# Optimization experiments

Hardware: AMD Instinct MI355X
Metric: run time of the kernel (lower is better)

## Reference

```python
import jax, jax.numpy as jnp
import numpy as np

B, S, H, L = 64, 512, 768, 9


def setup_inputs() -> dict:
    key = jax.random.key(0)
    ks = jax.random.split(key, 8)
    hidden = jax.random.normal(ks[0], (B, S, H), jnp.float32)
    lengths = jax.random.randint(ks[1], (B,), S // 2, S + 1)
    attention_mask = (jnp.arange(S)[None, :] < lengths[:, None]).astype(jnp.int32)
    labels = jax.random.randint(ks[2], (B, S), 0, L)
    # sprinkle some -100 ignore labels like HF datasets do
    ignore = jax.random.uniform(ks[3], (B, S)) < 0.05
    labels = jnp.where(ignore, -100, labels)
    W = jax.random.normal(ks[4], (H, L), jnp.float32) * 0.02
    b = jnp.zeros((L,), jnp.float32)
    start_transitions = jax.random.uniform(ks[5], (L,), jnp.float32, -0.1, 0.1)
    end_transitions = jax.random.uniform(ks[6], (L,), jnp.float32, -0.1, 0.1)
    transitions = jax.random.uniform(ks[7], (L, L), jnp.float32, -0.1, 0.1)
    return dict(hidden=hidden, attention_mask=attention_mask, labels=labels, W=W, b=b,
                start_transitions=start_transitions, end_transitions=end_transitions,
                transitions=transitions)


def _crf_numerator(emissions, tags, maskf, start_t, end_t, trans):
    # score of the gold tag sequence (torchcrf _compute_score)
    first = start_t[tags[:, 0]] + jnp.take_along_axis(emissions[:, 0], tags[:, 0:1], axis=1)[:, 0]
    em = jnp.take_along_axis(emissions, tags[..., None], axis=2)[..., 0]      # [B,S]
    tr = trans[tags[:, :-1], tags[:, 1:]]                                     # [B,S-1]
    score = first + jnp.sum((em[:, 1:] + tr) * maskf[:, 1:], axis=1)
    last_idx = (jnp.sum(maskf, axis=1).astype(jnp.int32) - 1)
    last_tags = jnp.take_along_axis(tags, last_idx[:, None], axis=1)[:, 0]
    return score + end_t[last_tags]


def _crf_lognorm(emissions, maskf, start_t, end_t, trans):
    # forward algorithm (torchcrf _compute_normalizer) as a lax.scan
    score0 = start_t[None, :] + emissions[:, 0]                               # [B,L]
    em_seq = jnp.transpose(emissions[:, 1:], (1, 0, 2))                       # [S-1,B,L]
    m_seq = maskf[:, 1:].T                                                    # [S-1,B]

    def step(score, xs):
        em_t, m_t = xs
        nxt = jax.nn.logsumexp(score[:, :, None] + trans[None] + em_t[:, None, :], axis=1)
        return jnp.where(m_t[:, None] > 0, nxt, score), None

    score, _ = jax.lax.scan(step, score0, (em_seq, m_seq))
    return jax.nn.logsumexp(score + end_t[None, :], axis=1)


def _viterbi(emissions, maskf, start_t, end_t, trans):
    score0 = start_t[None, :] + emissions[:, 0]                               # [B,L]
    em_seq = jnp.transpose(emissions[:, 1:], (1, 0, 2))
    m_seq = maskf[:, 1:].T

    def step(score, xs):
        em_t, m_t = xs
        cand = score[:, :, None] + trans[None]                                # [B,L,L]
        bp = jnp.argmax(cand, axis=1)                                         # [B,L]
        nxt = jnp.max(cand, axis=1) + em_t
        return jnp.where(m_t[:, None] > 0, nxt, score), bp

    score, history = jax.lax.scan(step, score0, (em_seq, m_seq))              # history [S-1,B,L]
    best_last = jnp.argmax(score + end_t[None, :], axis=1)                    # [B]

    def back(cur, xs):
        bp_t, m_t = xs
        prev = jnp.where(m_t > 0, jnp.take_along_axis(bp_t, cur[:, None], axis=1)[:, 0], cur)
        return prev, prev

    _, tags_rev = jax.lax.scan(back, best_last, (history[::-1], m_seq[::-1]))
    tags = jnp.concatenate([tags_rev[::-1].T, best_last[:, None]], axis=1)    # [B,S]
    return tags


def reference(hidden, attention_mask, labels, W, b, start_transitions, end_transitions, transitions):
    maskf = attention_mask.astype(hidden.dtype)                               # [B,S]
    logits = jnp.einsum('bsh,hl->bsl', hidden, W) + b                         # [B,S,L]
    safe_labels = jnp.where(labels == -100, 0, labels)
    num = _crf_numerator(logits, safe_labels, maskf, start_transitions, end_transitions, transitions)
    den = _crf_lognorm(logits, maskf, start_transitions, end_transitions, transitions)
    loss = -jnp.mean(num - den)                                               # -crf(..., reduction='mean')
    tags = _viterbi(logits, maskf, start_transitions, end_transitions, transitions)
    fake_logits = jax.nn.one_hot(tags, L, dtype=logits.dtype) * maskf[..., None]
    return loss, fake_logits
```

## Files before the change

kernel.cpp:

```cpp
#include <hip/hip_runtime.h>
#include <hip/hip_bf16.h>
#include <stdint.h>

constexpr int BB  = 64;
constexpr int SS  = 512;
constexpr int HH  = 768;
constexpr int NL  = 9;
constexpr int NROWS = BB * SS;
constexpr int EMN   = SS * NL;
constexpr int NSEG  = 8;
constexpr float NEG  = -1e30f;

__device__ __forceinline__ float readlane_f(float v, int lane) {
  union { float f; int i; } u;
  u.f = v;
  u.i = __builtin_amdgcn_readlane(u.i, lane);
  return u.f;
}

__device__ __forceinline__ float max3f(float a, float b, float c) {
  float d;
  asm("v_max3_f32 %0, %1, %2, %3" : "=v"(d) : "v"(a), "v"(b), "v"(c));
  return d;
}

__device__ __forceinline__ float max9f(const float* c) {
  return max3f(max3f(c[0], c[1], c[2]),
               max3f(c[3], c[4], c[5]),
               max3f(c[6], c[7], c[8]));
}

__global__ __launch_bounds__(256, 2) void logits_kernel(
    const float* __restrict__ hidden, const float* __restrict__ W,
    const float* __restrict__ bias, const int* __restrict__ mask,
    float* __restrict__ logits, int* __restrict__ lens,
    float* __restrict__ out) {
  const int lane = threadIdx.x & 63;
  const int wid  = blockIdx.x * 4 + (threadIdx.x >> 6);

  if (blockIdx.x == 0 && threadIdx.x == 0) out[0] = 0.0f;

  if (blockIdx.x < 64 && threadIdx.x < 64) {
    const int4* mp = (const int4*)(mask + blockIdx.x * SS);
    const int4 a = mp[threadIdx.x];
    const int4 c = mp[threadIdx.x + 64];
    int lsum = a.x + a.y + a.z + a.w + c.x + c.y + c.z + c.w;
#pragma unroll
    for (int off = 32; off >= 1; off >>= 1) lsum += __shfl_xor(lsum, off, 64);
    if (threadIdx.x == 0) lens[blockIdx.x] = lsum;
  }

  float w[3][4][NL];
#pragma unroll
  for (int j = 0; j < 3; ++j)
#pragma unroll
    for (int k = 0; k < 4; ++k) {
      const int r = lane * 4 + j * 256 + k;
#pragma unroll
      for (int l = 0; l < NL; ++l) w[j][k][l] = W[r * NL + l];
    }
  const float my_bias = (lane < NL) ? bias[lane] : 0.0f;

  float4 h[4][3];
#pragma unroll
  for (int r = 0; r < 4; ++r) {
    const float4* hp = (const float4*)(hidden + (size_t)(wid + r * 8192) * HH);
#pragma unroll
    for (int j = 0; j < 3; ++j) h[r][j] = hp[lane + j * 64];
  }
  float acc[4][NL];
#pragma unroll
  for (int r = 0; r < 4; ++r)
#pragma unroll
    for (int l = 0; l < NL; ++l) acc[r][l] = 0.0f;
#pragma unroll
  for (int r = 0; r < 4; ++r)
#pragma unroll
    for (int j = 0; j < 3; ++j)
#pragma unroll
      for (int l = 0; l < NL; ++l)
        acc[r][l] += h[r][j].x * w[j][0][l] + h[r][j].y * w[j][1][l] +
                     h[r][j].z * w[j][2][l] + h[r][j].w * w[j][3][l];
#pragma unroll
  for (int off = 32; off >= 1; off >>= 1)
#pragma unroll
    for (int r = 0; r < 4; ++r)
#pragma unroll
      for (int l = 0; l < NL; ++l)
        acc[r][l] += __shfl_xor(acc[r][l], off, 64);
  if (lane < NL) {
#pragma unroll
    for (int r = 0; r < 4; ++r) {
      float v = acc[r][0];
#pragma unroll
      for (int l = 1; l < NL; ++l) if (lane == l) v = acc[r][l];
      logits[(size_t)(wid + r * 8192) * NL + lane] = v + my_bias;
    }
  }
}

__global__ __launch_bounds__(64) void scan_kernel(
    const float* __restrict__ logits, const int* __restrict__ labels,
    const float* __restrict__ start_t, const float* __restrict__ end_t,
    const float* __restrict__ trans, float* __restrict__ out,
    float* __restrict__ num_den, const int* __restrict__ lens,
    float* __restrict__ segmat) {
  __shared__ uint32_t bpw[64 * NL];
  __shared__ unsigned char tags_s[SS];
  __shared__ unsigned char lab[SS];

  const int blk = blockIdx.x;
  const int tid = threadIdx.x;
  const int j   = (tid < NL) ? tid : NL - 1;

  if (blk < 64) {
    __builtin_amdgcn_s_setprio(1);
    const int b   = blk;
    const int len = lens[b];
    const float* emb = logits + (size_t)b * EMN;

    float tc[NL];
#pragma unroll
    for (int i = 0; i < NL; ++i) tc[i] = trans[i * NL + j];
    float s[NL];
#pragma unroll
    for (int i = 0; i < NL; ++i) s[i] = start_t[i] + emb[i];

    float e0[8], e1[8];
#pragma unroll
    for (int k = 0; k < 8; ++k) e0[k] = emb[(1 + k) * NL + j];

    for (int tb = 0; tb < 64; ++tb) {
      const int tbase = 8 * tb;
      if (tbase + 1 >= len) break;
      if (tb < 63) {
#pragma unroll
        for (int k = 0; k < 8; ++k) e1[k] = emb[(tbase + 9 + k) * NL + j];
      }
      uint32_t wpk = 0;
#pragma unroll
      for (int k = 0; k < 8; ++k) {
        const int t = tbase + 1 + k;
        if (t < len) {
          float c[NL];
#pragma unroll
          for (int i = 0; i < NL; ++i) c[i] = s[i] + tc[i];
          const float best = max9f(c);
          const float nxt  = best + e0[k];
          {
            const bool b01 = c[0] >= c[1], b23 = c[2] >= c[3];
            const bool b45 = c[4] >= c[5], b67 = c[6] >= c[7];
            const float v01 = b01 ? c[0] : c[1]; const int i01 = b01 ? 0 : 1;
            const float v23 = b23 ? c[2] : c[3]; const int i23 = b23 ? 2 : 3;
            const float v45 = b45 ? c[4] : c[5]; const int i45 = b45 ? 4 : 5;
            const float v67 = b67 ? c[6] : c[7]; const int i67 = b67 ? 6 : 7;
            const bool bA = v01 >= v23, bB = v45 >= v67;
            const float vA = bA ? v01 : v23; const int iA = bA ? i01 : i23;
            const float vB = bB ? v45 : v67; const int iB = bB ? i45 : i67;
            const bool bC = vA >= vB;
            const float vC = bC ? vA : vB; const int iC = bC ? iA : iB;
            const bool bD = vC >= c[8];
            const int arg = bD ? iC : 8;
            wpk |= (uint32_t)arg << (4 * k);
          }
#pragma unroll
          for (int i = 0; i < NL; ++i) s[i] = readlane_f(nxt, i);
        }
      }
      if (tid < NL) bpw[tb * NL + tid] = wpk;
#pragma unroll
      for (int k = 0; k < 8; ++k) e0[k] = e1[k];
    }
    float bv = s[0] + end_t[0];
    int   bl = 0;
#pragma unroll
    for (int i = 1; i < NL; ++i) {
      const float cc = s[i] + end_t[i];
      if (cc > bv) { bv = cc; bl = i; }
    }
    __syncthreads();

    uint32_t wv_[NL];
#pragma unroll
    for (int x = 0; x < NL; ++x) wv_[x] = bpw[tid * NL + x];
    uint64_t C = 0x876543210ULL;
#pragma unroll
    for (int k = 1; k <= 8; ++k) {
      const int t = 8 * tid + k;
      uint64_t nc = 0;
#pragma unroll
      for (int x = 0; x < 9; ++x) {
        const int g = (int)((wv_[x] >> (4 * (k - 1))) & 15u);
        nc |= ((C >> (4 * g)) & 15ULL) << (4 * x);
      }
      C = (t < len) ? nc : C;
    }
    const uint32_t Clo = (uint32_t)C, Chi = (uint32_t)(C >> 32);
    uint32_t cur = (uint32_t)bl;
    int bnd = 0;
#pragma unroll
    for (int c = 63; c >= 0; --c) {
      bnd = (tid == c) ? (int)cur : bnd;
      const uint32_t lo = (uint32_t)__builtin_amdgcn_readlane((int)Clo, c);
      const uint32_t hi = (uint32_t)__builtin_amdgcn_readlane((int)Chi, c);
      const uint64_t cc = ((uint64_t)hi << 32) | lo;
      cur = (uint32_t)((cc >> (4 * cur)) & 15u);
    }
    int tag = bnd;
#pragma unroll
    for (int k = 8; k >= 1; --k) {
      const int t = 8 * tid + k;
      const int tt = (t < 512) ? t : 511;
      const int blk2 = (tt - 1) >> 3;
      const int kk   = tt - 8 * blk2;
      const uint32_t bw = bpw[blk2 * NL + tag];
      const int nt = (int)((bw >> (4 * (kk - 1))) & 15u);
      tag = (t < len) ? nt : tag;
      tags_s[t - 1] = (unsigned char)tag;
    }
    __syncthreads();
    for (int i = tid; i < EMN; i += 64) {
      const int t = i / NL;
      const int l = i - t * NL;
      out[1 + (size_t)b * EMN + i] =
          (t < len && l == (int)tags_s[t]) ? 1.0f : 0.0f;
    }

  } else if (blk < 128) {
    const int b   = blk - 64;
    const int len = lens[b];
    const float* emb = logits + (size_t)b * EMN;
    for (int t = tid; t < SS; t += 64) {
      const int v = labels[b * SS + t];
      lab[t] = (unsigned char)((v == -100) ? 0 : v);
    }
    __syncthreads();
    float contrib = 0.0f;
    for (int t = tid; t < SS; t += 64) {
      if (t >= 1 && t < len)
        contrib += emb[t * NL + lab[t]] + trans[lab[t - 1] * NL + lab[t]];
    }
#pragma unroll
    for (int off = 32; off >= 1; off >>= 1)
      contrib += __shfl_xor(contrib, off, 64);
    if (tid == 0) {
      const int l0 = lab[0];
      num_den[b] = start_t[l0] + emb[l0] + contrib + end_t[lab[len - 1]];
    }

  } else {
    const int id   = blk - 128;
    const int pair = id / 3;
    const int wv   = id - pair * 3;
    const int b    = pair >> 3;
    const int sg   = pair & 7;
    const int e0   = 3 * wv;
    const int len  = lens[b];
    const float* emb = logits + (size_t)b * EMN;
    float tc[NL];
#pragma unroll
    for (int i = 0; i < NL; ++i) tc[i] = trans[i * NL + j];
    float s0[NL], s1[NL], s2[NL];
#pragma unroll
    for (int i = 0; i < NL; ++i) {
      s0[i] = (i == e0)     ? 0.0f : NEG;
      s1[i] = (i == e0 + 1) ? 0.0f : NEG;
      s2[i] = (i == e0 + 2) ? 0.0f : NEG;
    }
    float my0 = (j == e0)     ? 0.0f : NEG;
    float my1 = (j == e0 + 1) ? 0.0f : NEG;
    float my2 = (j == e0 + 2) ? 0.0f : NEG;
    const int tbeg  = 64 * sg + 1;
    const int tlast = (64 * sg + 64 < 511) ? 64 * sg + 64 : 511;
    float eA = emb[tbeg * NL + j],       eB = emb[(tbeg + 1) * NL + j];
    float eC = emb[(tbeg + 2) * NL + j], eD = emb[(tbeg + 3) * NL + j];
    for (int t = tbeg; t <= tlast; ++t) {
      if (t >= len) break;
      float c0[NL], c1[NL], c2[NL];
#pragma unroll
      for (int i = 0; i < NL; ++i) {
        c0[i] = s0[i] + tc[i];
        c1[i] = s1[i] + tc[i];
        c2[i] = s2[i] + tc[i];
      }
      const float m0 = max9f(c0);
      const float m1 = max9f(c1);
      const float m2 = max9f(c2);
      float u0 = 0.0f, u1 = 0.0f, u2 = 0.0f;
#pragma unroll
      for (int i = 0; i < NL; ++i) {
        u0 += __expf(c0[i] - m0);
        u1 += __expf(c1[i] - m1);
        u2 += __expf(c2[i] - m2);
      }
      my0 = m0 + __logf(u0) + eA;
      my1 = m1 + __logf(u1) + eA;
      my2 = m2 + __logf(u2) + eA;
#pragma unroll
      for (int i = 0; i < NL; ++i) {
        s0[i] = readlane_f(my0, i);
        s1[i] = readlane_f(my1, i);
        s2[i] = readlane_f(my2, i);
      }
      eA = eB; eB = eC; eC = eD;
      eD = emb[(t + 4) * NL + j];
    }
    if (tid < NL) {
      float* M = segmat + (size_t)(b * NSEG + sg) * 81;
      M[(e0    ) * NL + tid] = my0;
      M[(e0 + 1) * NL + tid] = my1;
      M[(e0 + 2) * NL + tid] = my2;
    }
  }
}

__global__ __launch_bounds__(64) void combine_kernel(
    const float* __restrict__ logits, const float* __restrict__ segmat,
    const float* __restrict__ start_t, const float* __restrict__ end_t,
    const float* __restrict__ num_den, float* __restrict__ out) {
  const int b   = blockIdx.x;
  const int tid = threadIdx.x;
  const int j   = (tid < NL) ? tid : NL - 1;
  float s[NL];
#pragma unroll
  for (int i = 0; i < NL; ++i) s[i] = start_t[i] + logits[(size_t)b * EMN + i];
  float mcur[NL], mnxt[NL];
  {
    const float* M = segmat + (size_t)(b * NSEG) * 81;
#pragma unroll
    for (int i = 0; i < NL; ++i) mcur[i] = M[i * NL + j];
  }
  for (int sg = 0; sg < NSEG; ++sg) {
    if (sg + 1 < NSEG) {
      const float* M = segmat + (size_t)(b * NSEG + sg + 1) * 81;
#pragma unroll
      for (int i = 0; i < NL; ++i) mnxt[i] = M[i * NL + j];
    }
    float c[NL];
#pragma unroll
    for (int i = 0; i < NL; ++i) c[i] = s[i] + mcur[i];
    const float m = max9f(c);
    float sum = 0.0f;
#pragma unroll
    for (int i = 0; i < NL; ++i) sum += __expf(c[i] - m);
    const float nxt = m + __logf(sum);
#pragma unroll
    for (int i = 0; i < NL; ++i) s[i] = readlane_f(nxt, i);
#pragma unroll
    for (int i = 0; i < NL; ++i) mcur[i] = mnxt[i];
  }
  float c[NL];
#pragma unroll
  for (int i = 0; i < NL; ++i) c[i] = s[i] + end_t[i];
  const float m = max9f(c);
  float sum = 0.0f;
#pragma unroll
  for (int i = 0; i < NL; ++i) sum += __expf(c[i] - m);
  if (tid == 0) {
    const float den = m + __logf(sum);
    atomicAdd(out, (den - num_den[b]) * (1.0f / 64.0f));
  }
}

extern "C" void kernel_launch(void* const* d_in, const int* in_sizes, int n_in,
                              void* d_out, int out_size, void* d_ws, size_t ws_size,
                              hipStream_t stream) {
  const float* hidden  = (const float*)d_in[0];
  const int*   mask    = (const int*)d_in[1];
  const int*   labels  = (const int*)d_in[2];
  const float* W       = (const float*)d_in[3];
  const float* bias    = (const float*)d_in[4];
  const float* start_t = (const float*)d_in[5];
  const float* end_t   = (const float*)d_in[6];
  const float* trans   = (const float*)d_in[7];
  float* out = (float*)d_out;

  float* logits  = (float*)d_ws;
  float* segmat  = logits + (size_t)NROWS * NL;
  float* num_den = segmat + (size_t)BB * NSEG * 81;
  int*   lens    = (int*)(num_den + 128);

  logits_kernel<<<2048, 256, 0, stream>>>(hidden, W, bias, mask, logits, lens, out);
  scan_kernel<<<1664, 64, 0, stream>>>(logits, labels, start_t, end_t, trans,
                                       out, num_den, lens, segmat);
  combine_kernel<<<64, 64, 0, stream>>>(logits, segmat, start_t, end_t,
                                        num_den, out);
}
```

Baseline: 240.9 us.

## Move Viterbi argmax off serial chain and fuse combine into scan via counters

The Viterbi forward loop now stores only the per-step max scores into shared memory, taking the argmax tree off the serial dependency chain. Backpointers are then recomputed in parallel across 63 lanes after the scan. The separate combine kernel is removed: a per-batch atomic counter lets the last finishing numerator or segment block run the logsumexp combine, saving a kernel launch. The cost is a large shared-memory buffer (about 23KB) that may lower occupancy for all 1664 blocks, plus fences and atomics.

```diff
diff --git a/kernel.cpp b/kernel.cpp
--- a/kernel.cpp
+++ b/kernel.cpp
@@ -30,15 +30,32 @@
                max3f(c[6], c[7], c[8]));
 }
 
+__device__ __forceinline__ int arg9(const float* c) {
+  const bool b01 = c[0] >= c[1], b23 = c[2] >= c[3];
+  const bool b45 = c[4] >= c[5], b67 = c[6] >= c[7];
+  const float v01 = b01 ? c[0] : c[1]; const int i01 = b01 ? 0 : 1;
+  const float v23 = b23 ? c[2] : c[3]; const int i23 = b23 ? 2 : 3;
+  const float v45 = b45 ? c[4] : c[5]; const int i45 = b45 ? 4 : 5;
+  const float v67 = b67 ? c[6] : c[7]; const int i67 = b67 ? 6 : 7;
+  const bool bA = v01 >= v23, bB = v45 >= v67;
+  const float vA = bA ? v01 : v23; const int iA = bA ? i01 : i23;
+  const float vB = bB ? v45 : v67; const int iB = bB ? i45 : i67;
+  const bool bC = vA >= vB;
+  const float vC = bC ? vA : vB; const int iC = bC ? iA : iB;
+  const bool bD = vC >= c[8];
+  return bD ? iC : 8;
+}
+
 __global__ __launch_bounds__(256, 2) void logits_kernel(
     const float* __restrict__ hidden, const float* __restrict__ W,
     const float* __restrict__ bias, const int* __restrict__ mask,
     float* __restrict__ logits, int* __restrict__ lens,
-    float* __restrict__ out) {
+    float* __restrict__ out, int* __restrict__ cnt) {
   const int lane = threadIdx.x & 63;
   const int wid  = blockIdx.x * 4 + (threadIdx.x >> 6);
 
   if (blockIdx.x == 0 && threadIdx.x == 0) out[0] = 0.0f;
+  if (blockIdx.x == 1 && threadIdx.x < BB) cnt[threadIdx.x] = 0;
 
   if (blockIdx.x < 64 && threadIdx.x < 64) {
     const int4* mp = (const int4*)(mask + blockIdx.x * SS);
@@ -99,15 +116,64 @@
   }
 }
 
+__device__ void combine_batch(int b, int tid,
+                              const float* __restrict__ logits,
+                              const float* __restrict__ segmat,
+                              const float* __restrict__ start_t,
+                              const float* __restrict__ end_t,
+                              const float* __restrict__ num_den,
+                              float* __restrict__ out) {
+  const int j = (tid < NL) ? tid : NL - 1;
+  float s[NL];
+#pragma unroll
+  for (int i = 0; i < NL; ++i) s[i] = start_t[i] + logits[(size_t)b * EMN + i];
+  float mcur[NL], mnxt[NL];
+  {
+    const float* M = segmat + (size_t)(b * NSEG) * 81;
+#pragma unroll
+    for (int i = 0; i < NL; ++i) mcur[i] = M[i * NL + j];
+  }
+  for (int sg = 0; sg < NSEG; ++sg) {
+    if (sg + 1 < NSEG) {
+      const float* M = segmat + (size_t)(b * NSEG + sg + 1) * 81;
+#pragma unroll
+      for (int i = 0; i < NL; ++i) mnxt[i] = M[i * NL + j];
+    }
+    float c[NL];
+#pragma unroll
+    for (int i = 0; i < NL; ++i) c[i] = s[i] + mcur[i];
+    const float m = max9f(c);
+    float sum = 0.0f;
+#pragma unroll
+    for (int i = 0; i < NL; ++i) sum += __expf(c[i] - m);
+    const float nxt = m + __logf(sum);
+#pragma unroll
+    for (int i = 0; i < NL; ++i) s[i] = readlane_f(nxt, i);
+#pragma unroll
+    for (int i = 0; i < NL; ++i) mcur[i] = mnxt[i];
+  }
+  float c[NL];
+#pragma unroll
+  for (int i = 0; i < NL; ++i) c[i] = s[i] + end_t[i];
+  const float m = max9f(c);
+  float sum = 0.0f;
+#pragma unroll
+  for (int i = 0; i < NL; ++i) sum += __expf(c[i] - m);
+  if (tid == 0) {
+    const float den = m + __logf(sum);
+    atomicAdd(out, (den - num_den[b]) * (1.0f / 64.0f));
+  }
+}
+
 __global__ __launch_bounds__(64) void scan_kernel(
     const float* __restrict__ logits, const int* __restrict__ labels,
     const float* __restrict__ start_t, const float* __restrict__ end_t,
     const float* __restrict__ trans, float* __restrict__ out,
     float* __restrict__ num_den, const int* __restrict__ lens,
-    float* __restrict__ segmat) {
-  __shared__ uint32_t bpw[64 * NL];
-  __shared__ unsigned char tags_s[SS];
-  __shared__ unsigned char lab[SS];
+    float* __restrict__ segmat, int* __restrict__ cnt) {
+  __shared__ float    straj[SS * NL];
+  __shared__ unsigned char bp_s[EMN];
+  __shared__ uint32_t tags_w[64];
 
   const int blk = blockIdx.x;
   const int tid = threadIdx.x;
@@ -122,22 +188,38 @@
     float tc[NL];
 #pragma unroll
     for (int i = 0; i < NL; ++i) tc[i] = trans[i * NL + j];
+
+    float slane = start_t[j] + emb[j];
+    straj[0 * NL + j] = slane;
     float s[NL];
 #pragma unroll
-    for (int i = 0; i < NL; ++i) s[i] = start_t[i] + emb[i];
+    for (int i = 0; i < NL; ++i) s[i] = readlane_f(slane, i);
 
     float e0[8], e1[8];
 #pragma unroll
     for (int k = 0; k < 8; ++k) e0[k] = emb[(1 + k) * NL + j];
 
-    for (int tb = 0; tb < 64; ++tb) {
+    const int nfull = (len - 1) >> 3;
+    for (int tb = 0; tb < nfull; ++tb) {
       const int tbase = 8 * tb;
-      if (tbase + 1 >= len) break;
-      if (tb < 63) {
-#pragma unroll
-        for (int k = 0; k < 8; ++k) e1[k] = emb[(tbase + 9 + k) * NL + j];
-      }
-      uint32_t wpk = 0;
+#pragma unroll
+      for (int k = 0; k < 8; ++k) e1[k] = emb[(tbase + 9 + k) * NL + j];
+#pragma unroll
+      for (int k = 0; k < 8; ++k) {
+        float c[NL];
+#pragma unroll
+        for (int i = 0; i < NL; ++i) c[i] = s[i] + tc[i];
+        const float best = max9f(c);
+        const float nxt  = best + e0[k];
+        straj[(tbase + 1 + k) * NL + j] = nxt;
+#pragma unroll
+        for (int i = 0; i < NL; ++i) s[i] = readlane_f(nxt, i);
+      }
+#pragma unroll
+      for (int k = 0; k < 8; ++k) e0[k] = e1[k];
+    }
+    {
+      const int tbase = 8 * nfull;
 #pragma unroll
       for (int k = 0; k < 8; ++k) {
         const int t = tbase + 1 + k;
@@ -147,29 +229,11 @@
           for (int i = 0; i < NL; ++i) c[i] = s[i] + tc[i];
           const float best = max9f(c);
           const float nxt  = best + e0[k];
-          {
-            const bool b01 = c[0] >= c[1], b23 = c[2] >= c[3];
-            const bool b45 = c[4] >= c[5], b67 = c[6] >= c[7];
-            const float v01 = b01 ? c[0] : c[1]; const int i01 = b01 ? 0 : 1;
-            const float v23 = b23 ? c[2] : c[3]; const int i23 = b23 ? 2 : 3;
-            const float v45 = b45 ? c[4] : c[5]; const int i45 = b45 ? 4 : 5;
-            const float v67 = b67 ? c[6] : c[7]; const int i67 = b67 ? 6 : 7;
-            const bool bA = v01 >= v23, bB = v45 >= v67;
-            const float vA = bA ? v01 : v23; const int iA = bA ? i01 : i23;
-            const float vB = bB ? v45 : v67; const int iB = bB ? i45 : i67;
-            const bool bC = vA >= vB;
-            const float vC = bC ? vA : vB; const int iC = bC ? iA : iB;
-            const bool bD = vC >= c[8];
-            const int arg = bD ? iC : 8;
-            wpk |= (uint32_t)arg << (4 * k);
-          }
+          straj[t * NL + j] = nxt;
 #pragma unroll
           for (int i = 0; i < NL; ++i) s[i] = readlane_f(nxt, i);
         }
       }
-      if (tid < NL) bpw[tb * NL + tid] = wpk;
-#pragma unroll
-      for (int k = 0; k < 8; ++k) e0[k] = e1[k];
     }
     float bv = s[0] + end_t[0];
     int   bl = 0;
@@ -178,20 +242,37 @@
       const float cc = s[i] + end_t[i];
       if (cc > bv) { bv = cc; bl = i; }
     }
+
+    {
+      const int g  = tid / 9;
+      const int jj = tid - 9 * g;
+      float tcol[NL];
+#pragma unroll
+      for (int i = 0; i < NL; ++i) tcol[i] = trans[i * NL + jj];
+      if (g < 7) {
+        for (int tt = 0; tt < 73; ++tt) {
+          const int t = 1 + g + 7 * tt;
+          if (t < len) {
+            float c[NL];
+#pragma unroll
+            for (int i = 0; i < NL; ++i) c[i] = straj[(t - 1) * NL + i] + tcol[i];
+            bp_s[t * NL + jj] = (unsigned char)arg9(c);
+          }
+        }
+      }
+    }
     __syncthreads();
 
-    uint32_t wv_[NL];
-#pragma unroll
-    for (int x = 0; x < NL; ++x) wv_[x] = bpw[tid * NL + x];
     uint64_t C = 0x876543210ULL;
 #pragma unroll
     for (int k = 1; k <= 8; ++k) {
-      const int t = 8 * tid + k;
+      const int t  = 8 * tid + k;
+      const int ti = (t < 512) ? t : 511;
       uint64_t nc = 0;
 #pragma unroll
       for (int x = 0; x < 9; ++x) {
-        const int g = (int)((wv_[x] >> (4 * (k - 1))) & 15u);
-        nc |= ((C >> (4 * g)) & 15ULL) << (4 * x);
+        const int g2 = bp_s[ti * NL + x] & 15;
+        nc |= ((C >> (4 * g2)) & 15ULL) << (4 * x);
       }
       C = (t < len) ? nc : C;
     }
@@ -207,29 +288,29 @@
       cur = (uint32_t)((cc >> (4 * cur)) & 15u);
     }
     int tag = bnd;
+    uint32_t tw = 0;
 #pragma unroll
     for (int k = 8; k >= 1; --k) {
-      const int t = 8 * tid + k;
-      const int tt = (t < 512) ? t : 511;
-      const int blk2 = (tt - 1) >> 3;
-      const int kk   = tt - 8 * blk2;
-      const uint32_t bw = bpw[blk2 * NL + tag];
-      const int nt = (int)((bw >> (4 * (kk - 1))) & 15u);
+      const int t  = 8 * tid + k;
+      const int ti = (t < 512) ? t : 511;
+      const int nt = bp_s[ti * NL + tag];
       tag = (t < len) ? nt : tag;
-      tags_s[t - 1] = (unsigned char)tag;
-    }
+      tw |= (uint32_t)tag << (4 * (k - 1));
+    }
+    tags_w[tid] = tw;
     __syncthreads();
     for (int i = tid; i < EMN; i += 64) {
       const int t = i / NL;
       const int l = i - t * NL;
-      out[1 + (size_t)b * EMN + i] =
-          (t < len && l == (int)tags_s[t]) ? 1.0f : 0.0f;
+      const int tg = (int)((tags_w[t >> 3] >> ((t & 7) * 4)) & 15u);
+      out[1 + (size_t)b * EMN + i] = (t < len && l == tg) ? 1.0f : 0.0f;
     }
 
   } else if (blk < 128) {
     const int b   = blk - 64;
     const int len = lens[b];
     const float* emb = logits + (size_t)b * EMN;
+    unsigned char* lab = (unsigned char*)straj;
     for (int t = tid; t < SS; t += 64) {
       const int v = labels[b * SS + t];
       lab[t] = (unsigned char)((v == -100) ? 0 : v);
@@ -246,6 +327,14 @@
     if (tid == 0) {
       const int l0 = lab[0];
       num_den[b] = start_t[l0] + emb[l0] + contrib + end_t[lab[len - 1]];
+    }
+    __threadfence();
+    int old = 0;
+    if (tid == 0) old = atomicAdd(&cnt[b], 1);
+    old = __builtin_amdgcn_readlane(old, 0);
+    if (old == 24) {
+      __threadfence();
+      combine_batch(b, tid, logits, segmat, start_t, end_t, num_den, out);
     }
 
   } else {
@@ -311,54 +400,14 @@
       M[(e0 + 1) * NL + tid] = my1;
       M[(e0 + 2) * NL + tid] = my2;
     }
-  }
-}
-
-__global__ __launch_bounds__(64) void combine_kernel(
-    const float* __restrict__ logits, const float* __restrict__ segmat,
-    const float* __restrict__ start_t, const float* __restrict__ end_t,
-    const float* __restrict__ num_den, float* __restrict__ out) {
-  const int b   = blockIdx.x;
-  const int tid = threadIdx.x;
-  const int j   = (tid < NL) ? tid : NL - 1;
-  float s[NL];
-#pragma unroll
-  for (int i = 0; i < NL; ++i) s[i] = start_t[i] + logits[(size_t)b * EMN + i];
-  float mcur[NL], mnxt[NL];
-  {
-    const float* M = segmat + (size_t)(b * NSEG) * 81;
-#pragma unroll
-    for (int i = 0; i < NL; ++i) mcur[i] = M[i * NL + j];
-  }
-  for (int sg = 0; sg < NSEG; ++sg) {
-    if (sg + 1 < NSEG) {
-      const float* M = segmat + (size_t)(b * NSEG + sg + 1) * 81;
-#pragma unroll
-      for (int i = 0; i < NL; ++i) mnxt[i] = M[i * NL + j];
-    }
-    float c[NL];
-#pragma unroll
-    for (int i = 0; i < NL; ++i) c[i] = s[i] + mcur[i];
-    const float m = max9f(c);
-    float sum = 0.0f;
-#pragma unroll
-    for (int i = 0; i < NL; ++i) sum += __expf(c[i] - m);
-    const float nxt = m + __logf(sum);
-#pragma unroll
-    for (int i = 0; i < NL; ++i) s[i] = readlane_f(nxt, i);
-#pragma unroll
-    for (int i = 0; i < NL; ++i) mcur[i] = mnxt[i];
-  }
-  float c[NL];
-#pragma unroll
-  for (int i = 0; i < NL; ++i) c[i] = s[i] + end_t[i];
-  const float m = max9f(c);
-  float sum = 0.0f;
-#pragma unroll
-  for (int i = 0; i < NL; ++i) sum += __expf(c[i] - m);
-  if (tid == 0) {
-    const float den = m + __logf(sum);
-    atomicAdd(out, (den - num_den[b]) * (1.0f / 64.0f));
+    __threadfence();
+    int old = 0;
+    if (tid == 0) old = atomicAdd(&cnt[b], 1);
+    old = __builtin_amdgcn_readlane(old, 0);
+    if (old == 24) {
+      __threadfence();
+      combine_batch(b, tid, logits, segmat, start_t, end_t, num_den, out);
+    }
   }
 }
 
@@ -379,10 +428,10 @@
   float* segmat  = logits + (size_t)NROWS * NL;
   float* num_den = segmat + (size_t)BB * NSEG * 81;
   int*   lens    = (int*)(num_den + 128);
-
-  logits_kernel<<<2048, 256, 0, stream>>>(hidden, W, bias, mask, logits, lens, out);
+  int*   cnt     = lens + 64;
+
+  logits_kernel<<<2048, 256, 0, stream>>>(hidden, W, bias, mask, logits, lens,
+                                          out, cnt);
   scan_kernel<<<1664, 64, 0, stream>>>(logits, labels, start_t, end_t, trans,
-                                       out, num_den, lens, segmat);
-  combine_kernel<<<64, 64, 0, stream>>>(logits, segmat, start_t, end_t,
-                                        num_den, out);
-}
+                                       out, num_den, lens, segmat, cnt);
+}
```

Result: slower. 248.1 us (+3.0%).

## Fold combine into scan blocks via last-block counter, split Viterbi kernel, restructure logits loads

Applied to the files above, without the earlier changes.

The separate combine kernel is removed. Each batch's forward-algorithm segment blocks and numerator block now bump an atomic counter, and the last block to finish runs the segment combine for that batch. Viterbi moves into its own small kernel launched after the rest, and the logits kernel now loads W and hidden per chunk with a higher occupancy bound, cutting register pressure. This relies on threadfence/atomic ordering and a counter reset in the logits kernel. It also serializes Viterbi after the forward scan instead of running them concurrently, which could lengthen the critical path.

```diff
diff --git a/kernel.cpp b/kernel.cpp
--- a/kernel.cpp
+++ b/kernel.cpp
@@ -30,15 +30,16 @@
                max3f(c[6], c[7], c[8]));
 }
 
-__global__ __launch_bounds__(256, 2) void logits_kernel(
+__global__ __launch_bounds__(256, 4) void logits_kernel(
     const float* __restrict__ hidden, const float* __restrict__ W,
     const float* __restrict__ bias, const int* __restrict__ mask,
     float* __restrict__ logits, int* __restrict__ lens,
-    float* __restrict__ out) {
+    float* __restrict__ out, int* __restrict__ cnt) {
   const int lane = threadIdx.x & 63;
   const int wid  = blockIdx.x * 4 + (threadIdx.x >> 6);
 
   if (blockIdx.x == 0 && threadIdx.x == 0) out[0] = 0.0f;
+  if (blockIdx.x == 1 && threadIdx.x < BB) cnt[threadIdx.x] = 0;
 
   if (blockIdx.x < 64 && threadIdx.x < 64) {
     const int4* mp = (const int4*)(mask + blockIdx.x * SS);
@@ -50,37 +51,37 @@
     if (threadIdx.x == 0) lens[blockIdx.x] = lsum;
   }
 
-  float w[3][4][NL];
-#pragma unroll
-  for (int j = 0; j < 3; ++j)
+  const float my_bias = (lane < NL) ? bias[lane] : 0.0f;
+
+  const float4* hp[4];
+#pragma unroll
+  for (int r = 0; r < 4; ++r)
+    hp[r] = (const float4*)(hidden + (size_t)(wid + r * 8192) * HH);
+
+  float acc[4][NL];
+#pragma unroll
+  for (int r = 0; r < 4; ++r)
+#pragma unroll
+    for (int l = 0; l < NL; ++l) acc[r][l] = 0.0f;
+
+#pragma unroll
+  for (int j = 0; j < 3; ++j) {
+    float w[4][NL];
 #pragma unroll
     for (int k = 0; k < 4; ++k) {
       const int r = lane * 4 + j * 256 + k;
 #pragma unroll
-      for (int l = 0; l < NL; ++l) w[j][k][l] = W[r * NL + l];
-    }
-  const float my_bias = (lane < NL) ? bias[lane] : 0.0f;
-
-  float4 h[4][3];
-#pragma unroll
-  for (int r = 0; r < 4; ++r) {
-    const float4* hp = (const float4*)(hidden + (size_t)(wid + r * 8192) * HH);
-#pragma unroll
-    for (int j = 0; j < 3; ++j) h[r][j] = hp[lane + j * 64];
-  }
-  float acc[4][NL];
-#pragma unroll
-  for (int r = 0; r < 4; ++r)
-#pragma unroll
-    for (int l = 0; l < NL; ++l) acc[r][l] = 0.0f;
-#pragma unroll
-  for (int r = 0; r < 4; ++r)
-#pragma unroll
-    for (int j = 0; j < 3; ++j)
+      for (int l = 0; l < NL; ++l) w[k][l] = W[r * NL + l];
+    }
+#pragma unroll
+    for (int r = 0; r < 4; ++r) {
+      const float4 h = hp[r][lane + j * 64];
 #pragma unroll
       for (int l = 0; l < NL; ++l)
-        acc[r][l] += h[r][j].x * w[j][0][l] + h[r][j].y * w[j][1][l] +
-                     h[r][j].z * w[j][2][l] + h[r][j].w * w[j][3][l];
+        acc[r][l] += h.x * w[0][l] + h.y * w[1][l] +
+                     h.z * w[2][l] + h.w * w[3][l];
+    }
+  }
 #pragma unroll
   for (int off = 32; off >= 1; off >>= 1)
 #pragma unroll
@@ -99,14 +100,61 @@
   }
 }
 
-__global__ __launch_bounds__(64) void scan_kernel(
+__device__ void combine_batch(int b, int tid,
+                              const float* __restrict__ logits,
+                              const float* __restrict__ segmat,
+                              const float* __restrict__ start_t,
+                              const float* __restrict__ end_t,
+                              const float* __restrict__ num_den,
+                              float* __restrict__ out) {
+  const int j = (tid < NL) ? tid : NL - 1;
+  float s[NL];
+#pragma unroll
+  for (int i = 0; i < NL; ++i) s[i] = start_t[i] + logits[(size_t)b * EMN + i];
+  float mcur[NL], mnxt[NL];
+  {
+    const float* M = segmat + (size_t)(b * NSEG) * 81;
+#pragma unroll
+    for (int i = 0; i < NL; ++i) mcur[i] = M[i * NL + j];
+  }
+  for (int sg = 0; sg < NSEG; ++sg) {
+    if (sg + 1 < NSEG) {
+      const float* M = segmat + (size_t)(b * NSEG + sg + 1) * 81;
+#pragma unroll
+      for (int i = 0; i < NL; ++i) mnxt[i] = M[i * NL + j];
+    }
+    float c[NL];
+#pragma unroll
+    for (int i = 0; i < NL; ++i) c[i] = s[i] + mcur[i];
+    const float m = max9f(c);
+    float sum = 0.0f;
+#pragma unroll
+    for (int i = 0; i < NL; ++i) sum += __expf(c[i] - m);
+    const float nxt = m + __logf(sum);
+#pragma unroll
+    for (int i = 0; i < NL; ++i) s[i] = readlane_f(nxt, i);
+#pragma unroll
+    for (int i = 0; i < NL; ++i) mcur[i] = mnxt[i];
+  }
+  float c[NL];
+#pragma unroll
+  for (int i = 0; i < NL; ++i) c[i] = s[i] + end_t[i];
+  const float m = max9f(c);
+  float sum = 0.0f;
+#pragma unroll
+  for (int i = 0; i < NL; ++i) sum += __expf(c[i] - m);
+  if (tid == 0) {
+    const float den = m + __logf(sum);
+    atomicAdd(out, (den - num_den[b]) * (1.0f / 64.0f));
+  }
+}
+
+__global__ __launch_bounds__(64) void rest_kernel(
     const float* __restrict__ logits, const int* __restrict__ labels,
     const float* __restrict__ start_t, const float* __restrict__ end_t,
     const float* __restrict__ trans, float* __restrict__ out,
     float* __restrict__ num_den, const int* __restrict__ lens,
-    float* __restrict__ segmat) {
-  __shared__ uint32_t bpw[64 * NL];
-  __shared__ unsigned char tags_s[SS];
+    float* __restrict__ segmat, int* __restrict__ cnt) {
   __shared__ unsigned char lab[SS];
 
   const int blk = blockIdx.x;
@@ -114,120 +162,7 @@
   const int j   = (tid < NL) ? tid : NL - 1;
 
   if (blk < 64) {
-    __builtin_amdgcn_s_setprio(1);
     const int b   = blk;
-    const int len = lens[b];
-    const float* emb = logits + (size_t)b * EMN;
-
-    float tc[NL];
-#pragma unroll
-    for (int i = 0; i < NL; ++i) tc[i] = trans[i * NL + j];
-    float s[NL];
-#pragma unroll
-    for (int i = 0; i < NL; ++i) s[i] = start_t[i] + emb[i];
-
-    float e0[8], e1[8];
-#pragma unroll
-    for (int k = 0; k < 8; ++k) e0[k] = emb[(1 + k) * NL + j];
-
-    for (int tb = 0; tb < 64; ++tb) {
-      const int tbase = 8 * tb;
-      if (tbase + 1 >= len) break;
-      if (tb < 63) {
-#pragma unroll
-        for (int k = 0; k < 8; ++k) e1[k] = emb[(tbase + 9 + k) * NL + j];
-      }
-      uint32_t wpk = 0;
-#pragma unroll
-      for (int k = 0; k < 8; ++k) {
-        const int t = tbase + 1 + k;
-        if (t < len) {
-          float c[NL];
-#pragma unroll
-          for (int i = 0; i < NL; ++i) c[i] = s[i] + tc[i];
-          const float best = max9f(c);
-          const float nxt  = best + e0[k];
-          {
-            const bool b01 = c[0] >= c[1], b23 = c[2] >= c[3];
-            const bool b45 = c[4] >= c[5], b67 = c[6] >= c[7];
-            const float v01 = b01 ? c[0] : c[1]; const int i01 = b01 ? 0 : 1;
-            const float v23 = b23 ? c[2] : c[3]; const int i23 = b23 ? 2 : 3;
-            const float v45 = b45 ? c[4] : c[5]; const int i45 = b45 ? 4 : 5;
-            const float v67 = b67 ? c[6] : c[7]; const int i67 = b67 ? 6 : 7;
-            const bool bA = v01 >= v23, bB = v45 >= v67;
-            const float vA = bA ? v01 : v23; const int iA = bA ? i01 : i23;
-            const float vB = bB ? v45 : v67; const int iB = bB ? i45 : i67;
-            const bool bC = vA >= vB;
-            const float vC = bC ? vA : vB; const int iC = bC ? iA : iB;
-            const bool bD = vC >= c[8];
-            const int arg = bD ? iC : 8;
-            wpk |= (uint32_t)arg << (4 * k);
-          }
-#pragma unroll
-          for (int i = 0; i < NL; ++i) s[i] = readlane_f(nxt, i);
-        }
-      }
-      if (tid < NL) bpw[tb * NL + tid] = wpk;
-#pragma unroll
-      for (int k = 0; k < 8; ++k) e0[k] = e1[k];
-    }
-    float bv = s[0] + end_t[0];
-    int   bl = 0;
-#pragma unroll
-    for (int i = 1; i < NL; ++i) {
-      const float cc = s[i] + end_t[i];
-      if (cc > bv) { bv = cc; bl = i; }
-    }
-    __syncthreads();
-
-    uint32_t wv_[NL];
-#pragma unroll
-    for (int x = 0; x < NL; ++x) wv_[x] = bpw[tid * NL + x];
-    uint64_t C = 0x876543210ULL;
-#pragma unroll
-    for (int k = 1; k <= 8; ++k) {
-      const int t = 8 * tid + k;
-      uint64_t nc = 0;
-#pragma unroll
-      for (int x = 0; x < 9; ++x) {
-        const int g = (int)((wv_[x] >> (4 * (k - 1))) & 15u);
-        nc |= ((C >> (4 * g)) & 15ULL) << (4 * x);
-      }
-      C = (t < len) ? nc : C;
-    }
-    const uint32_t Clo = (uint32_t)C, Chi = (uint32_t)(C >> 32);
-    uint32_t cur = (uint32_t)bl;
-    int bnd = 0;
-#pragma unroll
-    for (int c = 63; c >= 0; --c) {
-      bnd = (tid == c) ? (int)cur : bnd;
-      const uint32_t lo = (uint32_t)__builtin_amdgcn_readlane((int)Clo, c);
-      const uint32_t hi = (uint32_t)__builtin_amdgcn_readlane((int)Chi, c);
-      const uint64_t cc = ((uint64_t)hi << 32) | lo;
-      cur = (uint32_t)((cc >> (4 * cur)) & 15u);
-    }
-    int tag = bnd;
-#pragma unroll
-    for (int k = 8; k >= 1; --k) {
-      const int t = 8 * tid + k;
-      const int tt = (t < 512) ? t : 511;
-      const int blk2 = (tt - 1) >> 3;
-      const int kk   = tt - 8 * blk2;
-      const uint32_t bw = bpw[blk2 * NL + tag];
-      const int nt = (int)((bw >> (4 * (kk - 1))) & 15u);
-      tag = (t < len) ? nt : tag;
-      tags_s[t - 1] = (unsigned char)tag;
-    }
-    __syncthreads();
-    for (int i = tid; i < EMN; i += 64) {
-      const int t = i / NL;
-      const int l = i - t * NL;
-      out[1 + (size_t)b * EMN + i] =
-          (t < len && l == (int)tags_s[t]) ? 1.0f : 0.0f;
-    }
-
-  } else if (blk < 128) {
-    const int b   = blk - 64;
     const int len = lens[b];
     const float* emb = logits + (size_t)b * EMN;
     for (int t = tid; t < SS; t += 64) {
@@ -247,9 +182,17 @@
       const int l0 = lab[0];
       num_den[b] = start_t[l0] + emb[l0] + contrib + end_t[lab[len - 1]];
     }
+    __threadfence();
+    int old = 0;
+    if (tid == 0) old = atomicAdd(&cnt[b], 1);
+    old = __builtin_amdgcn_readlane(old, 0);
+    if (old == 24) {
+      __threadfence();
+      combine_batch(b, tid, logits, segmat, start_t, end_t, num_den, out);
+    }
 
   } else {
-    const int id   = blk - 128;
+    const int id   = blk - 64;
     const int pair = id / 3;
     const int wv   = id - pair * 3;
     const int b    = pair >> 3;
@@ -311,54 +254,137 @@
       M[(e0 + 1) * NL + tid] = my1;
       M[(e0 + 2) * NL + tid] = my2;
     }
-  }
-}
-
-__global__ __launch_bounds__(64) void combine_kernel(
-    const float* __restrict__ logits, const float* __restrict__ segmat,
-    const float* __restrict__ start_t, const float* __restrict__ end_t,
-    const float* __restrict__ num_den, float* __restrict__ out) {
-  const int b   = blockIdx.x;
+    __threadfence();
+    int old = 0;
+    if (tid == 0) old = atomicAdd(&cnt[b], 1);
+    old = __builtin_amdgcn_readlane(old, 0);
+    if (old == 24) {
+      __threadfence();
+      combine_batch(b, tid, logits, segmat, start_t, end_t, num_den, out);
+    }
+  }
+}
+
+__global__ __launch_bounds__(64) void viterbi_kernel(
+    const float* __restrict__ logits, const float* __restrict__ start_t,
+    const float* __restrict__ end_t, const float* __restrict__ trans,
+    float* __restrict__ out, const int* __restrict__ lens) {
+  __shared__ uint32_t bpw[64 * NL];
+  __shared__ unsigned char tags_s[SS];
+
   const int tid = threadIdx.x;
   const int j   = (tid < NL) ? tid : NL - 1;
+
+  __builtin_amdgcn_s_setprio(1);
+  const int b   = blockIdx.x;
+  const int len = lens[b];
+  const float* emb = logits + (size_t)b * EMN;
+
+  float tc[NL];
+#pragma unroll
+  for (int i = 0; i < NL; ++i) tc[i] = trans[i * NL + j];
   float s[NL];
 #pragma unroll
-  for (int i = 0; i < NL; ++i) s[i] = start_t[i] + logits[(size_t)b * EMN + i];
-  float mcur[NL], mnxt[NL];
-  {
-    const float* M = segmat + (size_t)(b * NSEG) * 81;
-#pragma unroll
-    for (int i = 0; i < NL; ++i) mcur[i] = M[i * NL + j];
-  }
-  for (int sg = 0; sg < NSEG; ++sg) {
-    if (sg + 1 < NSEG) {
-      const float* M = segmat + (size_t)(b * NSEG + sg + 1) * 81;
-#pragma unroll
-      for (int i = 0; i < NL; ++i) mnxt[i] = M[i * NL + j];
-    }
-    float c[NL];
-#pragma unroll
-    for (int i = 0; i < NL; ++i) c[i] = s[i] + mcur[i];
-    const float m = max9f(c);
-    float sum = 0.0f;
-#pragma unroll
-    for (int i = 0; i < NL; ++i) sum += __expf(c[i] - m);
-    const float nxt = m + __logf(sum);
-#pragma unroll
-    for (int i = 0; i < NL; ++i) s[i] = readlane_f(nxt, i);
-#pragma unroll
-    for (int i = 0; i < NL; ++i) mcur[i] = mnxt[i];
-  }
-  float c[NL];
-#pragma unroll
-  for (int i = 0; i < NL; ++i) c[i] = s[i] + end_t[i];
-  const float m = max9f(c);
-  float sum = 0.0f;
-#pragma unroll
-  for (int i = 0; i < NL; ++i) sum += __expf(c[i] - m);
-  if (tid == 0) {
-    const float den = m + __logf(sum);
-    atomicAdd(out, (den - num_den[b]) * (1.0f / 64.0f));
+  for (int i = 0; i < NL; ++i) s[i] = start_t[i] + emb[i];
+
+  float e0[8], e1[8];
+#pragma unroll
+  for (int k = 0; k < 8; ++k) e0[k] = emb[(1 + k) * NL + j];
+
+  for (int tb = 0; tb < 64; ++tb) {
+    const int tbase = 8 * tb;
+    if (tbase + 1 >= len) break;
+    if (tb < 63) {
+#pragma unroll
+      for (int k = 0; k < 8; ++k) e1[k] = emb[(tbase + 9 + k) * NL + j];
+    }
+    uint32_t wpk = 0;
+#pragma unroll
+    for (int k = 0; k < 8; ++k) {
+      const int t = tbase + 1 + k;
+      if (t < len) {
+        float c[NL];
+#pragma unroll
+        for (int i = 0; i < NL; ++i) c[i] = s[i] + tc[i];
+        const float best = max9f(c);
+        const float nxt  = best + e0[k];
+        {
+          const bool b01 = c[0] >= c[1], b23 = c[2] >= c[3];
+          const bool b45 = c[4] >= c[5], b67 = c[6] >= c[7];
+          const float v01 = b01 ? c[0] : c[1]; const int i01 = b01 ? 0 : 1;
+          const float v23 = b23 ? c[2] : c[3]; const int i23 = b23 ? 2 : 3;
+          const float v45 = b45 ? c[4] : c[5]; const int i45 = b45 ? 4 : 5;
+          const float v67 = b67 ? c[6] : c[7]; const int i67 = b67 ? 6 : 7;
+          const bool bA = v01 >= v23, bB = v45 >= v67;
+          const float vA = bA ? v01 : v23; const int iA = bA ? i01 : i23;
+          const float vB = bB ? v45 : v67; const int iB = bB ? i45 : i67;
+          const bool bC = vA >= vB;
+          const float vC = bC ? vA : vB; const int iC = bC ? iA : iB;
+          const bool bD = vC >= c[8];
+          const int arg = bD ? iC : 8;
+          wpk |= (uint32_t)arg << (4 * k);
+        }
+#pragma unroll
+        for (int i = 0; i < NL; ++i) s[i] = readlane_f(nxt, i);
+      }
+    }
+    if (tid < NL) bpw[tb * NL + tid] = wpk;
+#pragma unroll
+    for (int k = 0; k < 8; ++k) e0[k] = e1[k];
+  }
+  float bv = s[0] + end_t[0];
+  int   bl = 0;
+#pragma unroll
+  for (int i = 1; i < NL; ++i) {
+    const float cc = s[i] + end_t[i];
+    if (cc > bv) { bv = cc; bl = i; }
+  }
+  __syncthreads();
+
+  uint32_t wv_[NL];
+#pragma unroll
+  for (int x = 0; x < NL; ++x) wv_[x] = bpw[tid * NL + x];
+  uint64_t C = 0x876543210ULL;
+#pragma unroll
+  for (int k = 1; k <= 8; ++k) {
+    const int t = 8 * tid + k;
+    uint64_t nc = 0;
+#pragma unroll
+    for (int x = 0; x < 9; ++x) {
+      const int g = (int)((wv_[x] >> (4 * (k - 1))) & 15u);
+      nc |= ((C >> (4 * g)) & 15ULL) << (4 * x);
+    }
+    C = (t < len) ? nc : C;
+  }
+  const uint32_t Clo = (uint32_t)C, Chi = (uint32_t)(C >> 32);
+  uint32_t cur = (uint32_t)bl;
+  int bnd = 0;
+#pragma unroll
+  for (int c = 63; c >= 0; --c) {
+    bnd = (tid == c) ? (int)cur : bnd;
+    const uint32_t lo = (uint32_t)__builtin_amdgcn_readlane((int)Clo, c);
+    const uint32_t hi = (uint32_t)__builtin_amdgcn_readlane((int)Chi, c);
+    const uint64_t cc = ((uint64_t)hi << 32) | lo;
+    cur = (uint32_t)((cc >> (4 * cur)) & 15u);
+  }
+  int tag = bnd;
+#pragma unroll
+  for (int k = 8; k >= 1; --k) {
+    const int t = 8 * tid + k;
+    const int tt = (t < 512) ? t : 511;
+    const int blk2 = (tt - 1) >> 3;
+    const int kk   = tt - 8 * blk2;
+    const uint32_t bw = bpw[blk2 * NL + tag];
+    const int nt = (int)((bw >> (4 * (kk - 1))) & 15u);
+    tag = (t < len) ? nt : tag;
+    tags_s[t - 1] = (unsigned char)tag;
+  }
+  __syncthreads();
+  for (int i = tid; i < EMN; i += 64) {
+    const int t = i / NL;
+    const int l = i - t * NL;
+    out[1 + (size_t)b * EMN + i] =
+        (t < len && l == (int)tags_s[t]) ? 1.0f : 0.0f;
   }
 }
 
@@ -379,10 +405,12 @@
   float* segmat  = logits + (size_t)NROWS * NL;
   float* num_den = segmat + (size_t)BB * NSEG * 81;
   int*   lens    = (int*)(num_den + 128);
-
-  logits_kernel<<<2048, 256, 0, stream>>>(hidden, W, bias, mask, logits, lens, out);
-  scan_kernel<<<1664, 64, 0, stream>>>(logits, labels, start_t, end_t, trans,
-                                       out, num_den, lens, segmat);
-  combine_kernel<<<64, 64, 0, stream>>>(logits, segmat, start_t, end_t,
-                                        num_den, out);
-}
+  int*   cnt     = lens + 64;
+
+  logits_kernel<<<2048, 256, 0, stream>>>(hidden, W, bias, mask, logits, lens,
+                                          out, cnt);
+  rest_kernel<<<1600, 64, 0, stream>>>(logits, labels, start_t, end_t, trans,
+                                       out, num_den, lens, segmat, cnt);
+  viterbi_kernel<<<64, 64, 0, stream>>>(logits, start_t, end_t, trans,
+                                        out, lens);
+}
```

Measured after the change: 319.1 us. +32.4%, slower.
